# Performance work log

Hardware: AMD Instinct MI355X
Metric: run time of the kernel (lower is better)

The kernel has to match this reference:

```python
import jax, jax.numpy as jnp
import numpy as np

EPS = 1e-12  # torch F.normalize default eps


def setup_inputs() -> dict:
    key = jax.random.key(0)
    k1, k2, k3 = jax.random.split(key, 3)
    ns, d_in, n_feat, n_classes = 16384, 512, 256, 1000
    x = jax.random.normal(k1, (ns, d_in), dtype=jnp.float32)
    W = jax.random.normal(k2, (d_in, n_feat), dtype=jnp.float32) * 0.05
    # class prototypes: L2-normalized embeddings, one per seen class (seen_c == n_classes)
    means = jax.random.normal(k3, (n_classes, n_feat), dtype=jnp.float32)
    means = means / jnp.maximum(jnp.linalg.norm(means, axis=1, keepdims=True), EPS)
    return {"x": x, "W": W, "means": means, "t": 0}


def reference(x, W, means, t):
    # forward_training: backbone + L2 normalization along feature dim
    feats = x @ W                                   # [ns, n_feat]
    preds = feats / jnp.maximum(jnp.linalg.norm(feats, axis=1, keepdims=True), EPS)
    # deployment forward: nearest prototype by negative dot product
    # original: per-sample dist = -means @ pred^T; dist.min(0) -> class index
    dist = -(preds @ means.T)                       # [ns, seen_c]
    classpred = jnp.argmin(dist, axis=1)            # first min on ties, matches torch
    n_classes = means.shape[0]
    out = jax.nn.one_hot(classpred, n_classes, dtype=jnp.float32)  # [ns, n_classes]
    return out
```

## Files before the change

### kernel.cpp

```cpp
#include <hip/hip_runtime.h>
#include <float.h>

#define NS   16384
#define K1   512
#define F    256
#define NC   1000
#define SPB  64
#define NTHR 512
#define NBLK (NS / SPB)


typedef _Float16 half8  __attribute__((ext_vector_type(8)));
typedef _Float16 half4v __attribute__((ext_vector_type(4)));
typedef float    float4v __attribute__((ext_vector_type(4)));

#define M_OFF 262144

#define PREP_BLKS 192
#define ZERO_BLKS 2048

__global__ void prep(const float* __restrict__ W, const float* __restrict__ means,
                     _Float16* __restrict__ ws, float* __restrict__ out) {
    const int bid = blockIdx.x;
    if (bid >= PREP_BLKS) {
        const size_t total4 = (size_t)NS * NC / 4;
        const float4v z4 = (float4v){0.f, 0.f, 0.f, 0.f};
        size_t base = (size_t)(bid - PREP_BLKS) * 2048 + threadIdx.x;
#pragma unroll
        for (int j = 0; j < 8; ++j) {
            size_t q = base + (size_t)j * 256;
            if (q < total4)
                __builtin_nontemporal_store(z4, reinterpret_cast<float4v*>(out) + q);
        }
        return;
    }
    int g = bid * blockDim.x + threadIdx.x;
    if (g < 16384) {
        int lane = g & 63, tile = g >> 6;
        int ks = tile >> 4, nt = tile & 15;
        int k0 = ks * 32 + (lane >> 4) * 8;
        int n  = nt * 16 + (lane & 15);
        half8 hv, lv;
#pragma unroll
        for (int j = 0; j < 8; ++j) {
            float v = W[(size_t)(k0 + j) * F + n] * 16.0f;
            _Float16 hi = (_Float16)v;
            hv[j] = hi;
            lv[j] = (_Float16)(v - (float)hi);
        }
        _Float16* d = ws + (size_t)tile * 1024 + (size_t)lane * 8;
        *reinterpret_cast<half8*>(d)       = hv;
        *reinterpret_cast<half8*>(d + 512) = lv;
    } else {
        int gm = g - 16384;
        int lane = gm & 63, tile = gm >> 6;
        int ks = tile >> 6, gt = tile & 63;
        int k0 = ks * 32 + (lane >> 4) * 8;
        int c  = gt * 16 + (lane & 15);
        half8 hv, lv;
#pragma unroll
        for (int j = 0; j < 8; ++j) {
            float v = (c < NC) ? means[(size_t)c * F + k0 + j] * 16.0f : 0.0f;
            _Float16 hi = (_Float16)v;
            hv[j] = hi;
            lv[j] = (_Float16)(v - (float)hi);
        }
        _Float16* d = ws + M_OFF + (size_t)tile * 1024 + (size_t)lane * 8;
        *reinterpret_cast<half8*>(d)       = hv;
        *reinterpret_cast<half8*>(d + 512) = lv;
    }
}

#define MFMA(a, b, c) __builtin_amdgcn_mfma_f32_16x16x32_f16((a), (b), (c), 0, 0, 0)

__device__ __forceinline__ void vmwait(int n) {
    switch (n) {
        case 0: asm volatile("s_waitcnt vmcnt(0)" ::: "memory"); break;
        case 2: asm volatile("s_waitcnt vmcnt(2)" ::: "memory"); break;
        case 4: asm volatile("s_waitcnt vmcnt(4)" ::: "memory"); break;
        default: asm volatile("s_waitcnt vmcnt(6)" ::: "memory"); break;
    }
    __builtin_amdgcn_sched_barrier(0);
}

#define FH_OFF  0
#define FL_OFF  16896
#define OVL_OFF 33792
#define SH_HALVES (33792 + 32768)

__attribute__((amdgpu_flat_work_group_size(NTHR, NTHR), amdgpu_waves_per_eu(2, 4)))
__global__ void fused_mfma(const float* __restrict__ x,
                           const _Float16* __restrict__ ws,
                           float* __restrict__ out) {
    __shared__ _Float16 SH[SH_HALVES];
    __shared__ float cand_v[64][8];
    __shared__ int   cand_i[64][8];
    __shared__ int   bidx[64];

    const int tid  = threadIdx.x;
    const int lane = tid & 63;
    const int w    = tid >> 6;
    const int quad = lane >> 4;
    const int cl   = lane & 15;
    const int s0   = blockIdx.x * SPB;

    const int xrow = tid >> 3;
    const int xc4  = (tid & 7) * 4;

#define XSH(b,r,c) SH[OVL_OFF + (b)*2560 + (r)*40 + (c)]
#define XSL(b,r,c) SH[OVL_OFF + 5120 + (b)*2560 + (r)*40 + (c)]
#define FH(r,c)    SH[FH_OFF + (r)*264 + (c)]
#define FL(r,c)    SH[FL_OFF + (r)*264 + (c)]

    float4v acc1[2][4];
#pragma unroll
    for (int p = 0; p < 2; ++p)
#pragma unroll
        for (int mt = 0; mt < 4; ++mt)
            acc1[p][mt] = (float4v){0.f, 0.f, 0.f, 0.f};

    const _Float16* wsrc = ws + ((size_t)(w * 2) << 10) + ((size_t)lane << 3);
    half8 wbh[2][2], wbl[2][2];
#pragma unroll
    for (int p = 0; p < 2; ++p) {
        wbh[0][p] = *reinterpret_cast<const half8*>(wsrc + p * 1024);
        wbl[0][p] = *reinterpret_cast<const half8*>(wsrc + p * 1024 + 512);
    }

    float4v xv = *reinterpret_cast<const float4v*>(x + (size_t)(s0 + xrow) * K1 + xc4);

#pragma unroll
    for (int ks = 0; ks < 16; ++ks) {
        const int buf = ks & 1;
        {
            half4v hx, lx;
#pragma unroll
            for (int j = 0; j < 4; ++j) {
                float v = xv[j] * 8.0f;
                _Float16 hi = (_Float16)v;
                hx[j] = hi;
                lx[j] = (_Float16)(v - (float)hi);
            }
            *reinterpret_cast<half4v*>(&XSH(buf, xrow, xc4)) = hx;
            *reinterpret_cast<half4v*>(&XSL(buf, xrow, xc4)) = lx;
        }
        __syncthreads();
        if (ks < 15)
            xv = *reinterpret_cast<const float4v*>(
                x + (size_t)(s0 + xrow) * K1 + (ks + 1) * 32 + xc4);
        if (ks < 15) {
#pragma unroll
            for (int p = 0; p < 2; ++p) {
                wbh[buf ^ 1][p] = *reinterpret_cast<const half8*>(
                    wsrc + (size_t)(ks + 1) * 16384 + p * 1024);
                wbl[buf ^ 1][p] = *reinterpret_cast<const half8*>(
                    wsrc + (size_t)(ks + 1) * 16384 + p * 1024 + 512);
            }
        }
        half8 ah[4], al[4];
#pragma unroll
        for (int mt = 0; mt < 4; ++mt) {
            ah[mt] = *reinterpret_cast<const half8*>(&XSH(buf, mt * 16 + cl, quad * 8));
            al[mt] = *reinterpret_cast<const half8*>(&XSL(buf, mt * 16 + cl, quad * 8));
        }
#pragma unroll
        for (int p = 0; p < 2; ++p)
#pragma unroll
            for (int mt = 0; mt < 4; ++mt) {
                acc1[p][mt] = MFMA(ah[mt], wbh[buf][p], acc1[p][mt]);
                acc1[p][mt] = MFMA(ah[mt], wbl[buf][p], acc1[p][mt]);
                acc1[p][mt] = MFMA(al[mt], wbh[buf][p], acc1[p][mt]);
            }
    }

#pragma unroll
    for (int p = 0; p < 2; ++p)
#pragma unroll
        for (int mt = 0; mt < 4; ++mt)
#pragma unroll
            for (int r = 0; r < 4; ++r) {
                int srow = mt * 16 + quad * 4 + r;
                int n    = (w * 2 + p) * 16 + cl;
                float v  = acc1[p][mt][r];
                _Float16 hi = (_Float16)v;
                FH(srow, n) = hi;
                FL(srow, n) = (_Float16)(v - (float)hi);
            }
    __syncthreads();

    float4v acc2[4][8];
#pragma unroll
    for (int mt = 0; mt < 4; ++mt)
#pragma unroll
        for (int c = 0; c < 8; ++c)
            acc2[mt][c] = (float4v){0.f, 0.f, 0.f, 0.f};

    _Float16* fifo = &SH[OVL_OFF + w * 4096];
    const _Float16* mws = ws + M_OFF;

#define MT_G(i) (mws + (size_t)((((i) >> 3) << 6) + (((i) & 7) << 3) + w) * 1024 \
                     + (size_t)lane * 8)
#define STAGE(i) do {                                                          \
        const _Float16* g_ = MT_G(i);                                          \
        _Float16* l_ = fifo + ((i) & 3) * 1024;                                \
        __builtin_amdgcn_global_load_lds(                                      \
            (const __attribute__((address_space(1))) void*)g_,                 \
            (__attribute__((address_space(3))) void*)l_, 16, 0, 0);            \
        __builtin_amdgcn_global_load_lds(                                      \
            (const __attribute__((address_space(1))) void*)(g_ + 512),         \
            (__attribute__((address_space(3))) void*)(l_ + 512), 16, 0, 0);    \
    } while (0)

    half8 fah[4], fal[4];
    half8 fbh[2], fbl[2];

    STAGE(0); STAGE(1); STAGE(2);
    vmwait(4);
    fbh[0] = *reinterpret_cast<const half8*>(fifo + lane * 8);
    fbl[0] = *reinterpret_cast<const half8*>(fifo + 512 + lane * 8);

#pragma unroll
    for (int i = 0; i < 64; ++i) {
        if (i < 61) STAGE(i + 3);
        if (i < 61)      vmwait(4);
        else if (i == 61) vmwait(2);
        else if (i == 62) vmwait(0);
        if (i < 63) {
            const _Float16* sl = fifo + ((i + 1) & 3) * 1024 + lane * 8;
            fbh[(i + 1) & 1] = *reinterpret_cast<const half8*>(sl);
            fbl[(i + 1) & 1] = *reinterpret_cast<const half8*>(sl + 512);
        }
        if ((i & 7) == 0) {
            const int ks = i >> 3;
#pragma unroll
            for (int mt = 0; mt < 4; ++mt) {
                fah[mt] = *reinterpret_cast<const half8*>(
                    &FH(mt * 16 + cl, ks * 32 + quad * 8));
                fal[mt] = *reinterpret_cast<const half8*>(
                    &FL(mt * 16 + cl, ks * 32 + quad * 8));
            }
        }
        const int c = i & 7, rb = i & 1;
#pragma unroll
        for (int mt = 0; mt < 4; ++mt) {
            acc2[mt][c] = MFMA(fah[mt], fbh[rb], acc2[mt][c]);
            acc2[mt][c] = MFMA(fah[mt], fbl[rb], acc2[mt][c]);
            acc2[mt][c] = MFMA(fal[mt], fbh[rb], acc2[mt][c]);
        }
    }

#pragma unroll
    for (int mt = 0; mt < 4; ++mt)
#pragma unroll
        for (int r = 0; r < 4; ++r) {
            float v  = -FLT_MAX;
            int   ix = 0x7FFFFFFF;
#pragma unroll
            for (int nt = 0; nt < 8; ++nt) {
                int c = (nt * 8 + w) * 16 + cl;
                if (c < NC) {
                    float sc = acc2[mt][nt][r];
                    if (sc > v) { v = sc; ix = c; }
                }
            }
#pragma unroll
            for (int off = 1; off < 16; off <<= 1) {
                float ov = __shfl_xor(v, off, 64);
                int   oi = __shfl_xor(ix, off, 64);
                if (ov > v || (ov == v && oi < ix)) { v = ov; ix = oi; }
            }
            if (cl == 0) {
                int srow = mt * 16 + quad * 4 + r;
                cand_v[srow][w] = v;
                cand_i[srow][w] = ix;
            }
        }
    __syncthreads();

    if (tid < SPB) {
        float v  = cand_v[tid][0];
        int   ix = cand_i[tid][0];
#pragma unroll
        for (int q = 1; q < 8; ++q) {
            float ov = cand_v[tid][q];
            int   oi = cand_i[tid][q];
            if (ov > v || (ov == v && oi < ix)) { v = ov; ix = oi; }
        }
        bidx[tid] = ix;
    }
    __syncthreads();

    if (tid < SPB)
        out[(size_t)(s0 + tid) * NC + bidx[tid]] = 1.0f;
}

extern "C" void kernel_launch(void* const* d_in, const int* in_sizes, int n_in,
                              void* d_out, int out_size, void* d_ws, size_t ws_size,
                              hipStream_t stream) {
    const float* x     = (const float*)d_in[0];
    const float* W     = (const float*)d_in[1];
    const float* means = (const float*)d_in[2];
    float* out         = (float*)d_out;
    _Float16* ws       = (_Float16*)d_ws;

    prep<<<PREP_BLKS + ZERO_BLKS, 256, 0, stream>>>(W, means, ws, out);
    fused_mfma<<<NBLK, NTHR, 0, stream>>>(x, ws, out);
}
```

Measured before the change: 135.3 us.

## Swizzle LDS layouts, raise MFMA priority, and partially roll phase loops

Replaces the padded LDS layouts for the feature and x tiles with XOR-swizzled unpadded layouts to avoid bank conflicts while shrinking the shared footprint. MFMA blocks are wrapped in s_setprio raises so compute waves win issue arbitration over memory waves. The fully unrolled phase-1 and phase-2 loops are restructured into partially rolled outer loops with pointer increments, reducing code size and address arithmetic. Risks include incorrect swizzle addressing and changed scheduling from the rolled loops.

```diff
diff --git a/kernel.cpp b/kernel.cpp
--- a/kernel.cpp
+++ b/kernel.cpp
@@ -84,9 +84,15 @@
 }
 
 #define FH_OFF  0
-#define FL_OFF  16896
-#define OVL_OFF 33792
-#define SH_HALVES (33792 + 32768)
+#define FL_OFF  16384
+#define OVL_OFF 32768
+#define SH_HALVES 65536
+
+#define FH_P(r, c) (&SH[FH_OFF + ((r) << 8) + ((c) ^ (((r) & 7) << 3))])
+#define FL_P(r, c) (&SH[FL_OFF + ((r) << 8) + ((c) ^ (((r) & 7) << 3))])
+#define XS_IDX(r, c) ((((r) >> 1) << 6) + ((((((r) & 1) << 5)) + (c)) ^ ((((r) >> 1) & 7) << 3)))
+#define XSH_P(b, r, c) (&SH[OVL_OFF + (b) * 2048 + XS_IDX(r, c)])
+#define XSL_P(b, r, c) (&SH[OVL_OFF + 4096 + (b) * 2048 + XS_IDX(r, c)])
 
 __attribute__((amdgpu_flat_work_group_size(NTHR, NTHR), amdgpu_waves_per_eu(2, 4)))
 __global__ void fused_mfma(const float* __restrict__ x,
@@ -107,11 +113,6 @@
     const int xrow = tid >> 3;
     const int xc4  = (tid & 7) * 4;
 
-#define XSH(b,r,c) SH[OVL_OFF + (b)*2560 + (r)*40 + (c)]
-#define XSL(b,r,c) SH[OVL_OFF + 5120 + (b)*2560 + (r)*40 + (c)]
-#define FH(r,c)    SH[FH_OFF + (r)*264 + (c)]
-#define FL(r,c)    SH[FL_OFF + (r)*264 + (c)]
-
     float4v acc1[2][4];
 #pragma unroll
     for (int p = 0; p < 2; ++p)
@@ -129,48 +130,40 @@
 
     float4v xv = *reinterpret_cast<const float4v*>(x + (size_t)(s0 + xrow) * K1 + xc4);
 
-#pragma unroll
-    for (int ks = 0; ks < 16; ++ks) {
-        const int buf = ks & 1;
-        {
-            half4v hx, lx;
-#pragma unroll
-            for (int j = 0; j < 4; ++j) {
-                float v = xv[j] * 8.0f;
-                _Float16 hi = (_Float16)v;
-                hx[j] = hi;
-                lx[j] = (_Float16)(v - (float)hi);
-            }
-            *reinterpret_cast<half4v*>(&XSH(buf, xrow, xc4)) = hx;
-            *reinterpret_cast<half4v*>(&XSL(buf, xrow, xc4)) = lx;
-        }
-        __syncthreads();
-        if (ks < 15)
-            xv = *reinterpret_cast<const float4v*>(
-                x + (size_t)(s0 + xrow) * K1 + (ks + 1) * 32 + xc4);
-        if (ks < 15) {
-#pragma unroll
-            for (int p = 0; p < 2; ++p) {
-                wbh[buf ^ 1][p] = *reinterpret_cast<const half8*>(
-                    wsrc + (size_t)(ks + 1) * 16384 + p * 1024);
-                wbl[buf ^ 1][p] = *reinterpret_cast<const half8*>(
-                    wsrc + (size_t)(ks + 1) * 16384 + p * 1024 + 512);
-            }
-        }
-        half8 ah[4], al[4];
-#pragma unroll
-        for (int mt = 0; mt < 4; ++mt) {
-            ah[mt] = *reinterpret_cast<const half8*>(&XSH(buf, mt * 16 + cl, quad * 8));
-            al[mt] = *reinterpret_cast<const half8*>(&XSL(buf, mt * 16 + cl, quad * 8));
-        }
-#pragma unroll
-        for (int p = 0; p < 2; ++p)
-#pragma unroll
-            for (int mt = 0; mt < 4; ++mt) {
-                acc1[p][mt] = MFMA(ah[mt], wbh[buf][p], acc1[p][mt]);
-                acc1[p][mt] = MFMA(ah[mt], wbl[buf][p], acc1[p][mt]);
-                acc1[p][mt] = MFMA(al[mt], wbh[buf][p], acc1[p][mt]);
-            }
+#define P1_BODY(k, buf) do {                                                   \
+        { half4v hx, lx;                                                       \
+          _Pragma("unroll") for (int j = 0; j < 4; ++j) {                      \
+              float v = xv[j] * 8.0f; _Float16 hi = (_Float16)v;               \
+              hx[j] = hi; lx[j] = (_Float16)(v - (float)hi); }                 \
+          *reinterpret_cast<half4v*>(XSH_P(buf, xrow, xc4)) = hx;              \
+          *reinterpret_cast<half4v*>(XSL_P(buf, xrow, xc4)) = lx; }            \
+        __syncthreads();                                                       \
+        if ((k) < 15)                                                          \
+            xv = *reinterpret_cast<const float4v*>(                            \
+                x + (size_t)(s0 + xrow) * K1 + ((k) + 1) * 32 + xc4);          \
+        _Pragma("unroll") for (int p = 0; p < 2; ++p) {                        \
+            wbh[(buf) ^ 1][p] = *reinterpret_cast<const half8*>(               \
+                wsrc + (size_t)((k) + 1) * 16384 + p * 1024);                  \
+            wbl[(buf) ^ 1][p] = *reinterpret_cast<const half8*>(               \
+                wsrc + (size_t)((k) + 1) * 16384 + p * 1024 + 512); }          \
+        half8 ah[4], al[4];                                                    \
+        _Pragma("unroll") for (int mt = 0; mt < 4; ++mt) {                     \
+            ah[mt] = *reinterpret_cast<const half8*>(                          \
+                XSH_P(buf, mt * 16 + cl, quad * 8));                           \
+            al[mt] = *reinterpret_cast<const half8*>(                          \
+                XSL_P(buf, mt * 16 + cl, quad * 8)); }                         \
+        __builtin_amdgcn_s_setprio(1);                                         \
+        _Pragma("unroll") for (int p = 0; p < 2; ++p)                          \
+            _Pragma("unroll") for (int mt = 0; mt < 4; ++mt) {                 \
+                acc1[p][mt] = MFMA(ah[mt], wbh[buf][p], acc1[p][mt]);          \
+                acc1[p][mt] = MFMA(ah[mt], wbl[buf][p], acc1[p][mt]);          \
+                acc1[p][mt] = MFMA(al[mt], wbh[buf][p], acc1[p][mt]); }        \
+        __builtin_amdgcn_s_setprio(0);                                         \
+    } while (0)
+
+    for (int k2 = 0; k2 < 8; ++k2) {
+        P1_BODY(2 * k2, 0);
+        P1_BODY(2 * k2 + 1, 1);
     }
 
 #pragma unroll
@@ -183,8 +176,8 @@
                 int n    = (w * 2 + p) * 16 + cl;
                 float v  = acc1[p][mt][r];
                 _Float16 hi = (_Float16)v;
-                FH(srow, n) = hi;
-                FL(srow, n) = (_Float16)(v - (float)hi);
+                *FH_P(srow, n) = hi;
+                *FL_P(srow, n) = (_Float16)(v - (float)hi);
             }
     __syncthreads();
 
@@ -196,57 +189,69 @@
             acc2[mt][c] = (float4v){0.f, 0.f, 0.f, 0.f};
 
     _Float16* fifo = &SH[OVL_OFF + w * 4096];
-    const _Float16* mws = ws + M_OFF;
-
-#define MT_G(i) (mws + (size_t)((((i) >> 3) << 6) + (((i) & 7) << 3) + w) * 1024 \
-                     + (size_t)lane * 8)
-#define STAGE(i) do {                                                          \
-        const _Float16* g_ = MT_G(i);                                          \
-        _Float16* l_ = fifo + ((i) & 3) * 1024;                                \
+    const _Float16* mg = ws + M_OFF + ((size_t)w << 10) + ((size_t)lane << 3);
+
+#define STAGE_OFF(goff, slot) do {                                             \
         __builtin_amdgcn_global_load_lds(                                      \
-            (const __attribute__((address_space(1))) void*)g_,                 \
-            (__attribute__((address_space(3))) void*)l_, 16, 0, 0);            \
+            (const __attribute__((address_space(1))) void*)(mg + (goff)),      \
+            (__attribute__((address_space(3))) void*)(fifo + (slot) * 1024),   \
+            16, 0, 0);                                                         \
         __builtin_amdgcn_global_load_lds(                                      \
-            (const __attribute__((address_space(1))) void*)(g_ + 512),         \
-            (__attribute__((address_space(3))) void*)(l_ + 512), 16, 0, 0);    \
+            (const __attribute__((address_space(1))) void*)(mg + (goff) + 512),\
+            (__attribute__((address_space(3))) void*)(fifo + (slot) * 1024 + 512),\
+            16, 0, 0);                                                         \
+    } while (0)
+
+#define LOAD_A(kk) do { int c0_ = (kk) * 32 + quad * 8;                        \
+        _Pragma("unroll") for (int mt = 0; mt < 4; ++mt) {                     \
+            fah[mt] = *reinterpret_cast<const half8*>(FH_P(mt * 16 + cl, c0_));\
+            fal[mt] = *reinterpret_cast<const half8*>(FL_P(mt * 16 + cl, c0_));\
+        } } while (0)
+
+#define FB_READ(slot, rb) do {                                                 \
+        const _Float16* sl_ = fifo + (slot) * 1024 + lane * 8;                 \
+        fbh[rb] = *reinterpret_cast<const half8*>(sl_);                        \
+        fbl[rb] = *reinterpret_cast<const half8*>(sl_ + 512);                  \
+    } while (0)
+
+#define MFMA12(gt, rb) do {                                                    \
+        __builtin_amdgcn_s_setprio(1);                                         \
+        _Pragma("unroll") for (int mt = 0; mt < 4; ++mt) {                     \
+            acc2[mt][gt] = MFMA(fah[mt], fbh[rb], acc2[mt][gt]);               \
+            acc2[mt][gt] = MFMA(fah[mt], fbl[rb], acc2[mt][gt]);               \
+            acc2[mt][gt] = MFMA(fal[mt], fbh[rb], acc2[mt][gt]); }             \
+        __builtin_amdgcn_s_setprio(0);                                         \
     } while (0)
 
     half8 fah[4], fal[4];
     half8 fbh[2], fbl[2];
 
-    STAGE(0); STAGE(1); STAGE(2);
+    STAGE_OFF(0, 0); STAGE_OFF(8192, 1); STAGE_OFF(16384, 2);
+    LOAD_A(0);
     vmwait(4);
-    fbh[0] = *reinterpret_cast<const half8*>(fifo + lane * 8);
-    fbl[0] = *reinterpret_cast<const half8*>(fifo + 512 + lane * 8);
-
-#pragma unroll
-    for (int i = 0; i < 64; ++i) {
-        if (i < 61) STAGE(i + 3);
-        if (i < 61)      vmwait(4);
-        else if (i == 61) vmwait(2);
-        else if (i == 62) vmwait(0);
-        if (i < 63) {
-            const _Float16* sl = fifo + ((i + 1) & 3) * 1024 + lane * 8;
-            fbh[(i + 1) & 1] = *reinterpret_cast<const half8*>(sl);
-            fbl[(i + 1) & 1] = *reinterpret_cast<const half8*>(sl + 512);
-        }
-        if ((i & 7) == 0) {
-            const int ks = i >> 3;
-#pragma unroll
-            for (int mt = 0; mt < 4; ++mt) {
-                fah[mt] = *reinterpret_cast<const half8*>(
-                    &FH(mt * 16 + cl, ks * 32 + quad * 8));
-                fal[mt] = *reinterpret_cast<const half8*>(
-                    &FL(mt * 16 + cl, ks * 32 + quad * 8));
-            }
-        }
-        const int c = i & 7, rb = i & 1;
-#pragma unroll
-        for (int mt = 0; mt < 4; ++mt) {
-            acc2[mt][c] = MFMA(fah[mt], fbh[rb], acc2[mt][c]);
-            acc2[mt][c] = MFMA(fah[mt], fbl[rb], acc2[mt][c]);
-            acc2[mt][c] = MFMA(fal[mt], fbh[rb], acc2[mt][c]);
-        }
+    FB_READ(0, 0);
+
+    for (int ks = 0; ks < 7; ++ks) {
+#pragma unroll
+        for (int gt = 0; gt < 8; ++gt) {
+            if (gt < 5) STAGE_OFF((gt + 3) * 8192, (gt + 3) & 3);
+            else        STAGE_OFF(65536 + (gt - 5) * 8192, (gt + 3) & 3);
+            if (gt == 0 && ks > 0) LOAD_A(ks);
+            vmwait(4);
+            FB_READ((gt + 1) & 3, (gt + 1) & 1);
+            MFMA12(gt, gt & 1);
+        }
+        mg += 65536;
+    }
+#pragma unroll
+    for (int gt = 0; gt < 8; ++gt) {
+        if (gt < 5) STAGE_OFF((gt + 3) * 8192, (gt + 3) & 3);
+        if (gt == 0) LOAD_A(7);
+        if (gt < 5)       vmwait(4);
+        else if (gt == 5) vmwait(2);
+        else if (gt == 6) vmwait(0);
+        if (gt < 7) FB_READ((gt + 1) & 3, (gt + 1) & 1);
+        MFMA12(gt, gt & 1);
     }
 
 #pragma unroll
```

Measured after the change: 138.5 us. 2.4% more time.

## Stage x directly into LDS with async loads, swizzle feature LDS, add MFMA priority

Applied to the files above, without the earlier changes.

The first GEMM now loads fp32 x tiles straight into LDS through global_load_lds with a 4-deep ring, and does the fp16 hi/lo split after reading from LDS instead of before writing. A __syncthreads is replaced by a raw s_barrier paired with vmcnt waits. The padded feature buffers become XOR-swizzled to avoid bank conflicts without padding, and s_setprio raises wave priority around the MFMA blocks. This aims to remove register round-trips and barrier stalls from the x staging. The cost is more complex manual synchronisation that could race if the vmcnt counting is wrong.

```diff
diff --git a/kernel.cpp b/kernel.cpp
--- a/kernel.cpp
+++ b/kernel.cpp
@@ -11,7 +11,6 @@
 
 
 typedef _Float16 half8  __attribute__((ext_vector_type(8)));
-typedef _Float16 half4v __attribute__((ext_vector_type(4)));
 typedef float    float4v __attribute__((ext_vector_type(4)));
 
 #define M_OFF 262144
@@ -78,15 +77,20 @@
         case 0: asm volatile("s_waitcnt vmcnt(0)" ::: "memory"); break;
         case 2: asm volatile("s_waitcnt vmcnt(2)" ::: "memory"); break;
         case 4: asm volatile("s_waitcnt vmcnt(4)" ::: "memory"); break;
+        case 5: asm volatile("s_waitcnt vmcnt(5)" ::: "memory"); break;
         default: asm volatile("s_waitcnt vmcnt(6)" ::: "memory"); break;
     }
     __builtin_amdgcn_sched_barrier(0);
 }
+#define SBAR() asm volatile("s_barrier" ::: "memory")
 
 #define FH_OFF  0
-#define FL_OFF  16896
-#define OVL_OFF 33792
-#define SH_HALVES (33792 + 32768)
+#define FL_OFF  16384
+#define OVL_OFF 32768
+#define SH_HALVES 65536
+
+#define FH_P(r, c) (&SH[FH_OFF + ((r) << 8) + ((c) ^ (((r) & 7) << 3))])
+#define FL_P(r, c) (&SH[FL_OFF + ((r) << 8) + ((c) ^ (((r) & 7) << 3))])
 
 __attribute__((amdgpu_flat_work_group_size(NTHR, NTHR), amdgpu_waves_per_eu(2, 4)))
 __global__ void fused_mfma(const float* __restrict__ x,
@@ -104,13 +108,7 @@
     const int cl   = lane & 15;
     const int s0   = blockIdx.x * SPB;
 
-    const int xrow = tid >> 3;
-    const int xc4  = (tid & 7) * 4;
-
-#define XSH(b,r,c) SH[OVL_OFF + (b)*2560 + (r)*40 + (c)]
-#define XSL(b,r,c) SH[OVL_OFF + 5120 + (b)*2560 + (r)*40 + (c)]
-#define FH(r,c)    SH[FH_OFF + (r)*264 + (c)]
-#define FL(r,c)    SH[FL_OFF + (r)*264 + (c)]
+    char* xlds = reinterpret_cast<char*>(&SH[OVL_OFF]);
 
     float4v acc1[2][4];
 #pragma unroll
@@ -127,50 +125,63 @@
         wbl[0][p] = *reinterpret_cast<const half8*>(wsrc + p * 1024 + 512);
     }
 
-    float4v xv = *reinterpret_cast<const float4v*>(x + (size_t)(s0 + xrow) * K1 + xc4);
-
-#pragma unroll
-    for (int ks = 0; ks < 16; ++ks) {
-        const int buf = ks & 1;
-        {
-            half4v hx, lx;
-#pragma unroll
-            for (int j = 0; j < 4; ++j) {
-                float v = xv[j] * 8.0f;
+    const float* xsrc = x + (size_t)(s0 + w * 8 + (lane >> 3)) * K1
+                          + (((lane & 7) ^ (lane >> 3)) << 2);
+
+#define XSTAGE(kk) __builtin_amdgcn_global_load_lds(                           \
+        (const __attribute__((address_space(1))) void*)(xsrc + (kk) * 32),     \
+        (__attribute__((address_space(3))) void*)                              \
+            (xlds + (((kk) & 3) * 8192) + w * 1024), 16, 0, 0)
+
+    XSTAGE(0);
+    XSTAGE(1);
+
+#pragma unroll
+    for (int k = 0; k < 16; ++k) {
+        if (k < 15) {
+#pragma unroll
+            for (int p = 0; p < 2; ++p) {
+                wbh[(k + 1) & 1][p] = *reinterpret_cast<const half8*>(
+                    wsrc + (size_t)(k + 1) * 16384 + p * 1024);
+                wbl[(k + 1) & 1][p] = *reinterpret_cast<const half8*>(
+                    wsrc + (size_t)(k + 1) * 16384 + p * 1024 + 512);
+            }
+        }
+        if (k < 14) XSTAGE(k + 2);
+        if (k < 14)      vmwait(6);
+        else if (k == 14) vmwait(5);
+        else              vmwait(0);
+        SBAR();
+
+        float4v xa[4][2];
+#pragma unroll
+        for (int mt = 0; mt < 4; ++mt) {
+            const char* rb = xlds + (k & 3) * 8192 + (mt * 16 + cl) * 128;
+            xa[mt][0] = *reinterpret_cast<const float4v*>(
+                rb + (((quad * 2)     ^ (cl & 7)) * 16));
+            xa[mt][1] = *reinterpret_cast<const float4v*>(
+                rb + (((quad * 2 + 1) ^ (cl & 7)) * 16));
+        }
+        half8 ah[4], al[4];
+#pragma unroll
+        for (int mt = 0; mt < 4; ++mt)
+#pragma unroll
+            for (int j = 0; j < 8; ++j) {
+                float v = xa[mt][j >> 2][j & 3] * 8.0f;
                 _Float16 hi = (_Float16)v;
-                hx[j] = hi;
-                lx[j] = (_Float16)(v - (float)hi);
-            }
-            *reinterpret_cast<half4v*>(&XSH(buf, xrow, xc4)) = hx;
-            *reinterpret_cast<half4v*>(&XSL(buf, xrow, xc4)) = lx;
-        }
-        __syncthreads();
-        if (ks < 15)
-            xv = *reinterpret_cast<const float4v*>(
-                x + (size_t)(s0 + xrow) * K1 + (ks + 1) * 32 + xc4);
-        if (ks < 15) {
-#pragma unroll
-            for (int p = 0; p < 2; ++p) {
-                wbh[buf ^ 1][p] = *reinterpret_cast<const half8*>(
-                    wsrc + (size_t)(ks + 1) * 16384 + p * 1024);
-                wbl[buf ^ 1][p] = *reinterpret_cast<const half8*>(
-                    wsrc + (size_t)(ks + 1) * 16384 + p * 1024 + 512);
-            }
-        }
-        half8 ah[4], al[4];
-#pragma unroll
-        for (int mt = 0; mt < 4; ++mt) {
-            ah[mt] = *reinterpret_cast<const half8*>(&XSH(buf, mt * 16 + cl, quad * 8));
-            al[mt] = *reinterpret_cast<const half8*>(&XSL(buf, mt * 16 + cl, quad * 8));
-        }
+                ah[mt][j] = hi;
+                al[mt][j] = (_Float16)(v - (float)hi);
+            }
+        __builtin_amdgcn_s_setprio(1);
 #pragma unroll
         for (int p = 0; p < 2; ++p)
 #pragma unroll
             for (int mt = 0; mt < 4; ++mt) {
-                acc1[p][mt] = MFMA(ah[mt], wbh[buf][p], acc1[p][mt]);
-                acc1[p][mt] = MFMA(ah[mt], wbl[buf][p], acc1[p][mt]);
-                acc1[p][mt] = MFMA(al[mt], wbh[buf][p], acc1[p][mt]);
-            }
+                acc1[p][mt] = MFMA(ah[mt], wbh[k & 1][p], acc1[p][mt]);
+                acc1[p][mt] = MFMA(ah[mt], wbl[k & 1][p], acc1[p][mt]);
+                acc1[p][mt] = MFMA(al[mt], wbh[k & 1][p], acc1[p][mt]);
+            }
+        __builtin_amdgcn_s_setprio(0);
     }
 
 #pragma unroll
@@ -183,8 +194,8 @@
                 int n    = (w * 2 + p) * 16 + cl;
                 float v  = acc1[p][mt][r];
                 _Float16 hi = (_Float16)v;
-                FH(srow, n) = hi;
-                FL(srow, n) = (_Float16)(v - (float)hi);
+                *FH_P(srow, n) = hi;
+                *FL_P(srow, n) = (_Float16)(v - (float)hi);
             }
     __syncthreads();
 
@@ -235,18 +246,20 @@
 #pragma unroll
             for (int mt = 0; mt < 4; ++mt) {
                 fah[mt] = *reinterpret_cast<const half8*>(
-                    &FH(mt * 16 + cl, ks * 32 + quad * 8));
+                    FH_P(mt * 16 + cl, ks * 32 + quad * 8));
                 fal[mt] = *reinterpret_cast<const half8*>(
-                    &FL(mt * 16 + cl, ks * 32 + quad * 8));
+                    FL_P(mt * 16 + cl, ks * 32 + quad * 8));
             }
         }
         const int c = i & 7, rb = i & 1;
+        __builtin_amdgcn_s_setprio(1);
 #pragma unroll
         for (int mt = 0; mt < 4; ++mt) {
             acc2[mt][c] = MFMA(fah[mt], fbh[rb], acc2[mt][c]);
             acc2[mt][c] = MFMA(fah[mt], fbl[rb], acc2[mt][c]);
             acc2[mt][c] = MFMA(fal[mt], fbh[rb], acc2[mt][c]);
         }
+        __builtin_amdgcn_s_setprio(0);
     }
 
 #pragma unroll
```

Measured after the change: 137.6 us. Within noise of the previous version (+1.7%).
